# Performance work log

Measured on AMD Instinct MI355X. Metric: run time of the kernel, lower is better.

The kernel has to match this reference:

```python
import jax, jax.numpy as jnp
import numpy as np

ALPHA = 0.2  # LeakyReLU negative slope
NEG_INF = -1.0e12


def setup_inputs() -> dict:
    key = jax.random.key(0)
    ks = jax.random.split(key, 8)
    N, F, D, H, M, Q = 4096, 512, 64, 4, 2, 128
    x = jax.random.normal(ks[0], (N, F), dtype=jnp.float32)
    adj = jax.random.randint(ks[1], (M, N, N), 0, 2, dtype=jnp.int32)
    W = jax.random.normal(ks[2], (H, F, D), dtype=jnp.float32) * 0.07
    a1 = jax.random.normal(ks[3], (H, D), dtype=jnp.float32) * 0.15
    a2 = jax.random.normal(ks[4], (H, D), dtype=jnp.float32) * 0.15
    Ws = jax.random.normal(ks[5], (H * D, Q), dtype=jnp.float32) * 0.1
    bs = jax.random.normal(ks[6], (1, Q), dtype=jnp.float32) * 0.1
    q_sem = jax.random.normal(ks[7], (Q, 1), dtype=jnp.float32) * 0.15
    return {"x": x, "adj": adj, "W": W, "a1": a1, "a2": a2,
            "Ws": Ws, "bs": bs, "q_sem": q_sem}


def reference(x, adj, W, a1, a2, Ws, bs, q_sem):
    N = x.shape[0]
    # Wh is identical across meta-paths (dropout disabled / eval mode)
    Wh = jnp.einsum('nf,hfd->hnd', x, W)            # [H,N,D]
    s1 = jnp.einsum('hnd,hd->hn', Wh, a1)           # Wh @ a[:D]
    s2 = jnp.einsum('hnd,hd->hn', Wh, a2)           # Wh @ a[D:]

    def metapath(adj_m):
        # e[h,i,j] = leaky_relu(s1[h,i] + s2[h,j]); mask by adjacency
        e = jax.nn.leaky_relu(s1[:, :, None] + s2[:, None, :], negative_slope=ALPHA)
        e = jnp.where(adj_m[None, :, :] > 0, e, NEG_INF)
        att = jax.nn.softmax(e, axis=2)             # softmax over neighbors (dim=1 in torch [N,N])
        h = jax.nn.elu(jnp.einsum('hnm,hmd->hnd', att, Wh))
        return jnp.transpose(h, (1, 0, 2)).reshape(N, -1)  # concat heads -> [N, H*D]

    Z = jax.vmap(metapath)(adj)                     # [M, N, H*D]
    z = jnp.transpose(Z, (1, 0, 2))                 # [N, M, H*D]

    # Semantic attention (faithful to original, incl. softmax over dim=1 of [M,1])
    Whs = jnp.tanh(jnp.einsum('nmf,fq->nmq', z, Ws) + bs)   # [N,M,Q]
    w = jnp.einsum('nmq,qo->nmo', Whs, q_sem).mean(0)        # [M,1]
    beta = jax.nn.softmax(w, axis=1)                          # [M,1]
    return (beta[None, :, :] * z).sum(axis=1)                 # [N, H*D]
```

## Files before the change

### kernel.cpp

```cpp
#include <hip/hip_runtime.h>
#include <hip/hip_fp16.h>
#include <stdint.h>

#define NN 4096
#define FF 512
#define DD 64
#define HH 4
#define MM 2
#define LOG2E 1.44269504088896340736f
#define ALPHA_LR 0.2f

typedef float f32x4 __attribute__((ext_vector_type(4)));
typedef _Float16 f16x8 __attribute__((ext_vector_type(8)));
typedef _Float16 f16x2 __attribute__((ext_vector_type(2)));

extern "C" __device__ _Float16 __ocml_exp2_f16(_Float16);

union H4 { ushort4 u; _Float16 h[4]; };
union W8 { f16x8 v; uint32_t w[4]; f16x2 p[4]; };

__device__ inline float fast_exp2(float x) { return __builtin_amdgcn_exp2f(x); }
__device__ inline float fast_rcp(float x) { return __builtin_amdgcn_rcpf(x); }
__device__ inline f32x4 mfma16(f16x8 a, f16x8 b, f32x4 c) {
    return __builtin_amdgcn_mfma_f32_16x16x32_f16(a, b, c, 0, 0, 0);
}
__device__ inline uint32_t enc_f32(float f) {
    uint32_t u = __float_as_uint(f);
    return (u & 0x80000000u) ? ~u : (u | 0x80000000u);
}
__device__ inline float dec_f32(uint32_t k) {
    uint32_t u = (k & 0x80000000u) ? (k ^ 0x80000000u) : ~k;
    return __uint_as_float(u);
}
__device__ inline uint32_t mpair(uint32_t rs, int k) {
    return (((rs >> (2 * k)) & 1u) ? 0x0000FFFFu : 0u) |
           (((rs >> (2 * k + 1)) & 1u) ? 0xFFFF0000u : 0u);
}

__global__ __launch_bounds__(256) void k_prep(const float* __restrict__ x,
                                              const int* __restrict__ adj,
                                              const float* __restrict__ W,
                                              _Float16* __restrict__ xh,
                                              _Float16* __restrict__ wt,
                                              unsigned long long* __restrict__ bitsT,
                                              uint32_t* __restrict__ m4a) {
    const int bid = blockIdx.x;
    if (bid < 2048) {
        const long long total = (long long)MM * NN * NN;
        const long long stride = 2048LL * 256;
        long long tid = (long long)bid * 256 + threadIdx.x;
        for (long long e = tid; e < total; e += stride) {
            unsigned long long msk = __ballot(adj[e] != 0);
            if ((threadIdx.x & 63) == 0) {
                long long q = e >> 6;
                int m  = (int)(q >> 18);
                int rem = (int)(q & 262143);
                int i  = rem >> 6;
                int jw = rem & 63;
                bitsT[((size_t)m * 64 + jw) * NN + i] = msk;
            }
        }
    } else if (bid < 4096) {
        int t = (bid - 2048) * 256 + threadIdx.x;
        if (t < HH) m4a[t] = 0u;
        float4 v = ((const float4*)x)[t];
        H4 o;
        o.h[0] = (_Float16)v.x; o.h[1] = (_Float16)v.y;
        o.h[2] = (_Float16)v.z; o.h[3] = (_Float16)v.w;
        ((ushort4*)xh)[t] = o.u;
    } else {
        int t = (bid - 4096) * 256 + threadIdx.x;
        int c = t >> 9, f = t & 511;
        int h = c >> 6, d = c & 63;
        wt[t] = (_Float16)W[(h * FF + f) * DD + d];
    }
}

__global__ __launch_bounds__(512) void k_wh(const _Float16* __restrict__ xh,
                                            const _Float16* __restrict__ wt,
                                            const float* __restrict__ a1,
                                            const float* __restrict__ a2,
                                            _Float16* __restrict__ whT,
                                            float* __restrict__ s1L,
                                            _Float16* __restrict__ s2h,
                                            uint32_t* __restrict__ m4a) {
    __shared__ float sred[8][2][16];
    const int wave = threadIdx.x >> 6;
    const int h    = wave & 3;
    const int th   = wave >> 2;
    const int lane = threadIdx.x & 63;
    const int iL   = lane & 15;
    const int quad = lane >> 4;
    const int i0   = blockIdx.x * 16;

    f32x4 acc[2];
    acc[0] = (f32x4){0.f, 0.f, 0.f, 0.f};
    acc[1] = (f32x4){0.f, 0.f, 0.f, 0.f};

    const _Float16* arow  = xh + (size_t)(i0 + iL) * FF + quad * 8;
    const _Float16* bbase = wt + (size_t)(h * 64 + th * 32 + iL) * FF + quad * 8;

    for (int kc = 0; kc < FF; kc += 32) {
        f16x8 a = *(const f16x8*)(arow + kc);
        #pragma unroll
        for (int u = 0; u < 2; ++u) {
            f16x8 b = *(const f16x8*)(bbase + (size_t)(16 * u) * FF + kc);
            acc[u] = mfma16(a, b, acc[u]);
        }
    }
    #pragma unroll
    for (int u = 0; u < 2; ++u) {
        H4 o;
        #pragma unroll
        for (int r = 0; r < 4; ++r) o.h[r] = (_Float16)acc[u][r];
        *(ushort4*)(whT + (size_t)(h * 64 + th * 32 + 16 * u + iL) * NN + i0 + quad * 4) = o.u;
    }

    const float a1v0 = a1[h * 64 + th * 32 + iL];
    const float a1v1 = a1[h * 64 + th * 32 + 16 + iL];
    const float a2v0 = a2[h * 64 + th * 32 + iL];
    const float a2v1 = a2[h * 64 + th * 32 + 16 + iL];
    #pragma unroll
    for (int r = 0; r < 4; ++r) {
        float p1 = acc[0][r] * a1v0 + acc[1][r] * a1v1;
        float p2 = acc[0][r] * a2v0 + acc[1][r] * a2v1;
        #pragma unroll
        for (int off = 1; off < 16; off <<= 1) {
            p1 += __shfl_xor(p1, off);
            p2 += __shfl_xor(p2, off);
        }
        if (iL == 0) {
            sred[wave][0][quad * 4 + r] = p1;
            sred[wave][1][quad * 4 + r] = p2;
        }
    }
    __syncthreads();
    if (threadIdx.x < 64) {
        int h2  = threadIdx.x >> 4;
        int idx = threadIdx.x & 15;
        float s1 = sred[h2][0][idx] + sred[h2 + 4][0][idx];
        float s2 = sred[h2][1][idx] + sred[h2 + 4][1][idx];
        float s2l = s2 * LOG2E;
        s1L[h2 * NN + i0 + idx] = s1 * LOG2E;
        s2h[h2 * NN + i0 + idx] = (_Float16)s2l;
        float mx = s2l;
        #pragma unroll
        for (int off = 1; off < 16; off <<= 1) mx = fmaxf(mx, __shfl_xor(mx, off));
        if (idx == 0) atomicMax(m4a + h2, enc_f32(mx));
    }
}

__global__ __launch_bounds__(512, 2) void k_attn(const _Float16* __restrict__ whT,
                                                 const float* __restrict__ s1L,
                                                 const _Float16* __restrict__ s2h,
                                                 const uint32_t* __restrict__ m4a,
                                                 const unsigned long long* __restrict__ bitsT,
                                                 float* __restrict__ out) {
    __shared__ __align__(16) float xr[4][MM][4][16][16];
    __shared__ __align__(16) float dr[4][MM][16];

    const int tid  = threadIdx.x;
    const int wave = tid >> 6;
    const int lane = tid & 63;
    const int iL   = lane & 15;
    const int quad = lane >> 4;
    const int h    = blockIdx.x & 3;
    const int i0   = (blockIdx.x >> 2) * 64;

    const float m4 = dec_f32(m4a[h]);
    f16x2 A2[4], B2[4];
    #pragma unroll
    for (int s = 0; s < 4; ++s) {
        float s1i = s1L[h * NN + i0 + 16 * s + iL];
        float vv  = s1i + m4;
        float cii = fmaxf(vv, ALPHA_LR * vv);
        _Float16 a = (_Float16)(s1i - cii);
        _Float16 b = (_Float16)(ALPHA_LR * s1i - cii);
        A2[s] = (f16x2){a, a};
        B2[s] = (f16x2){b, b};
    }
    const f16x2 al2 = (f16x2){(_Float16)ALPHA_LR, (_Float16)ALPHA_LR};

    f32x4 acc[4][MM][4];
    f32x4 accD[4][MM];
    #pragma unroll
    for (int s = 0; s < 4; ++s)
        #pragma unroll
        for (int m = 0; m < MM; ++m) {
            accD[s][m] = (f32x4){0.f, 0.f, 0.f, 0.f};
            #pragma unroll
            for (int t = 0; t < 4; ++t) acc[s][m][t] = (f32x4){0.f, 0.f, 0.f, 0.f};
        }

    f16x8 bones;
    #pragma unroll
    for (int e = 0; e < 8; ++e) bones[e] = (_Float16)1.0f;

    const _Float16* s2row = s2h + h * NN;
    const _Float16* brow = whT + (size_t)(h * 64 + iL) * NN;
    const int qshift = quad * 8;
    const int jbase = wave * 512;

    const unsigned long long* pB[MM][4];
    #pragma unroll
    for (int m = 0; m < MM; ++m)
        #pragma unroll
        for (int s = 0; s < 4; ++s)
            pB[m][s] = bitsT + (size_t)m * 64 * NN + i0 + 16 * s + iL;

    for (int it = 0; it < 8; ++it) {
        const int jc = jbase + it * 64;
        const int jw = jc >> 6;
        unsigned long long bm[MM][4];
        #pragma unroll
        for (int m = 0; m < MM; ++m)
            #pragma unroll
            for (int s = 0; s < 4; ++s)
                bm[m][s] = pB[m][s][(size_t)jw * NN];

        #pragma unroll
        for (int half = 0; half < 2; ++half) {
            const int jb = jc + 32 * half;
            f16x8 bfr[4];
            #pragma unroll
            for (int t = 0; t < 4; ++t)
                bfr[t] = *(const f16x8*)(brow + (size_t)(16 * t) * NN + jb + qshift);

            const W8 s2v = *(const W8*)(s2row + jb + qshift);
            const int shft = 32 * half + qshift;

            #pragma unroll
            for (int s = 0; s < 4; ++s) {
                uint32_t rs0 = (uint32_t)(bm[0][s] >> shft);
                uint32_t rs1 = (uint32_t)(bm[1][s] >> shft);
                W8 a0, a1v;
                #pragma unroll
                for (int k = 0; k < 4; ++k) {
                    f16x2 z = s2v.p[k] + A2[s];
                    f16x2 l = al2 * s2v.p[k] + B2[s];
                    _Float16 m0 = z[0] > l[0] ? z[0] : l[0];
                    _Float16 m1 = z[1] > l[1] ? z[1] : l[1];
                    f16x2 p = (f16x2){__ocml_exp2_f16(m0), __ocml_exp2_f16(m1)};
                    uint32_t pw = __builtin_bit_cast(uint32_t, p);
                    a0.w[k]  = pw & mpair(rs0, k);
                    a1v.w[k] = pw & mpair(rs1, k);
                }
                #pragma unroll
                for (int t = 0; t < 4; ++t) {
                    acc[s][0][t] = mfma16(a0.v, bfr[t], acc[s][0][t]);
                    acc[s][1][t] = mfma16(a1v.v, bfr[t], acc[s][1][t]);
                }
                accD[s][0] = mfma16(a0.v, bones, accD[s][0]);
                accD[s][1] = mfma16(a1v.v, bones, accD[s][1]);
            }
        }
    }

    #define STORE_SLOT(sl, s)                                                 \
        { _Pragma("unroll") for (int m = 0; m < MM; ++m) {                    \
              _Pragma("unroll") for (int t = 0; t < 4; ++t)                   \
                  *(f32x4*)&xr[sl][m][t][iL][quad * 4] = acc[s][m][t];        \
              if (iL == 0) *(f32x4*)&dr[sl][m][quad * 4] = accD[s][m]; } }
    #define ADD_SLOT(sl, s)                                                   \
        { _Pragma("unroll") for (int m = 0; m < MM; ++m) {                    \
              _Pragma("unroll") for (int t = 0; t < 4; ++t)                   \
                  acc[s][m][t] += *(const f32x4*)&xr[sl][m][t][iL][quad * 4]; \
              accD[s][m] += *(const f32x4*)&dr[sl][m][quad * 4]; } }

    for (int s = 0; s < 4; ++s) {
        __syncthreads();
        if (wave >= 4) STORE_SLOT(wave - 4, s);
        __syncthreads();
        if (wave < 4) ADD_SLOT(wave, s);
        __syncthreads();
        if (wave >= 2 && wave < 4) STORE_SLOT(wave - 2, s);
        __syncthreads();
        if (wave < 2) ADD_SLOT(wave, s);
        __syncthreads();
        if (wave == 1) STORE_SLOT(0, s);
        __syncthreads();
        if (wave == 0) {
            ADD_SLOT(0, s);
            const int i0s = i0 + 16 * s;
            #pragma unroll
            for (int t = 0; t < 4; ++t) {
                #pragma unroll
                for (int r = 0; r < 4; ++r) {
                    float v0 = acc[s][0][t][r] * fast_rcp(accD[s][0][r]);
                    float v1 = acc[s][1][t][r] * fast_rcp(accD[s][1][r]);
                    float e0 = v0 > 0.f ? v0 : (fast_exp2(v0 * LOG2E) - 1.f);
                    float e1 = v1 > 0.f ? v1 : (fast_exp2(v1 * LOG2E) - 1.f);
                    out[(size_t)(i0s + quad * 4 + r) * (HH * DD) + h * 64 + 16 * t + iL] = e0 + e1;
                }
            }
        }
    }
    #undef STORE_SLOT
    #undef ADD_SLOT
}

extern "C" void kernel_launch(void* const* d_in, const int* in_sizes, int n_in,
                              void* d_out, int out_size, void* d_ws, size_t ws_size,
                              hipStream_t stream) {
    const float* x   = (const float*)d_in[0];
    const int*   adj = (const int*)d_in[1];
    const float* W   = (const float*)d_in[2];
    const float* a1  = (const float*)d_in[3];
    const float* a2  = (const float*)d_in[4];
    float* out = (float*)d_out;

    char* ws = (char*)d_ws;
    _Float16* xh   = (_Float16*)(ws);
    _Float16* wt   = (_Float16*)(ws + 4194304);
    _Float16* whT  = (_Float16*)(ws + 4456448);
    float*    s1L  = (float*)(ws + 6553600);
    _Float16* s2h  = (_Float16*)(ws + 6619136);
    uint32_t* m4a  = (uint32_t*)(ws + 6684672);
    unsigned long long* bitsT = (unsigned long long*)(ws + 6750208);

    hipLaunchKernelGGL(k_prep, dim3(4608), dim3(256), 0, stream,
                       x, adj, W, xh, wt, bitsT, m4a);
    hipLaunchKernelGGL(k_wh, dim3(256), dim3(512), 0, stream,
                       xh, wt, a1, a2, whT, s1L, s2h, m4a);
    hipLaunchKernelGGL(k_attn, dim3(256), dim3(512), 0, stream,
                       whT, s1L, s2h, m4a, bitsT, out);
}
```

Before: 276.1 us.

## Packed f16 max and mask-multiply, single-pass LDS cross-wave reduction

The inner loop now applies the adjacency mask by multiplying with packed 0/1 half values built from shifted bits, and uses a packed f16 max, replacing scalar selects and per-element AND masks. The epilogue changes from a tree reduction over waves with six barriers per slot to a single pass. All eight waves write their partials to a larger LDS buffer, and four waves each sum one output tile. This cuts barriers and serialized reduction work but doubles the LDS used for the reduction buffer, which may affect occupancy.

```diff
diff --git a/kernel.cpp b/kernel.cpp
--- a/kernel.cpp
+++ b/kernel.cpp
@@ -13,6 +13,7 @@
 typedef float f32x4 __attribute__((ext_vector_type(4)));
 typedef _Float16 f16x8 __attribute__((ext_vector_type(8)));
 typedef _Float16 f16x2 __attribute__((ext_vector_type(2)));
+typedef unsigned short u16x2 __attribute__((ext_vector_type(2)));
 
 extern "C" __device__ _Float16 __ocml_exp2_f16(_Float16);
 
@@ -32,9 +33,17 @@
     uint32_t u = (k & 0x80000000u) ? (k ^ 0x80000000u) : ~k;
     return __uint_as_float(u);
 }
-__device__ inline uint32_t mpair(uint32_t rs, int k) {
-    return (((rs >> (2 * k)) & 1u) ? 0x0000FFFFu : 0u) |
-           (((rs >> (2 * k + 1)) & 1u) ? 0xFFFF0000u : 0u);
+__device__ inline f16x2 msk01(uint32_t V, int k) {
+    uint32_t w = (V >> (2 * k)) & 0x00010001u;
+    u16x2 m = __builtin_bit_cast(u16x2, w) * (u16x2){0x3C00, 0x3C00};
+    return __builtin_bit_cast(f16x2, m);
+}
+__device__ inline f16x2 pkmax(f16x2 a, f16x2 b) {
+#if __has_builtin(__builtin_elementwise_max)
+    return __builtin_elementwise_max(a, b);
+#else
+    return (f16x2){a[0] > b[0] ? a[0] : b[0], a[1] > b[1] ? a[1] : b[1]};
+#endif
 }
 
 __global__ __launch_bounds__(256) void k_prep(const float* __restrict__ x,
@@ -156,8 +165,8 @@
                                                  const uint32_t* __restrict__ m4a,
                                                  const unsigned long long* __restrict__ bitsT,
                                                  float* __restrict__ out) {
-    __shared__ __align__(16) float xr[4][MM][4][16][16];
-    __shared__ __align__(16) float dr[4][MM][16];
+    __shared__ __align__(16) float xr[8][MM][4][16][16];
+    __shared__ __align__(16) float dr[8][MM][16];
 
     const int tid  = threadIdx.x;
     const int wave = tid >> 6;
@@ -231,19 +240,19 @@
 
             #pragma unroll
             for (int s = 0; s < 4; ++s) {
-                uint32_t rs0 = (uint32_t)(bm[0][s] >> shft);
-                uint32_t rs1 = (uint32_t)(bm[1][s] >> shft);
+                uint32_t rs0 = (uint32_t)(bm[0][s] >> shft) & 0xFFu;
+                uint32_t rs1 = (uint32_t)(bm[1][s] >> shft) & 0xFFu;
+                uint32_t V0 = rs0 | (rs0 << 15);
+                uint32_t V1 = rs1 | (rs1 << 15);
                 W8 a0, a1v;
                 #pragma unroll
                 for (int k = 0; k < 4; ++k) {
                     f16x2 z = s2v.p[k] + A2[s];
                     f16x2 l = al2 * s2v.p[k] + B2[s];
-                    _Float16 m0 = z[0] > l[0] ? z[0] : l[0];
-                    _Float16 m1 = z[1] > l[1] ? z[1] : l[1];
-                    f16x2 p = (f16x2){__ocml_exp2_f16(m0), __ocml_exp2_f16(m1)};
-                    uint32_t pw = __builtin_bit_cast(uint32_t, p);
-                    a0.w[k]  = pw & mpair(rs0, k);
-                    a1v.w[k] = pw & mpair(rs1, k);
+                    f16x2 mx = pkmax(z, l);
+                    f16x2 p = (f16x2){__ocml_exp2_f16(mx[0]), __ocml_exp2_f16(mx[1])};
+                    a0.p[k]  = p * msk01(V0, k);
+                    a1v.p[k] = p * msk01(V1, k);
                 }
                 #pragma unroll
                 for (int t = 0; t < 4; ++t) {
@@ -256,47 +265,40 @@
         }
     }
 
-    #define STORE_SLOT(sl, s)                                                 \
-        { _Pragma("unroll") for (int m = 0; m < MM; ++m) {                    \
-              _Pragma("unroll") for (int t = 0; t < 4; ++t)                   \
-                  *(f32x4*)&xr[sl][m][t][iL][quad * 4] = acc[s][m][t];        \
-              if (iL == 0) *(f32x4*)&dr[sl][m][quad * 4] = accD[s][m]; } }
-    #define ADD_SLOT(sl, s)                                                   \
-        { _Pragma("unroll") for (int m = 0; m < MM; ++m) {                    \
-              _Pragma("unroll") for (int t = 0; t < 4; ++t)                   \
-                  acc[s][m][t] += *(const f32x4*)&xr[sl][m][t][iL][quad * 4]; \
-              accD[s][m] += *(const f32x4*)&dr[sl][m][quad * 4]; } }
-
     for (int s = 0; s < 4; ++s) {
         __syncthreads();
-        if (wave >= 4) STORE_SLOT(wave - 4, s);
+        #pragma unroll
+        for (int m = 0; m < MM; ++m) {
+            #pragma unroll
+            for (int t = 0; t < 4; ++t)
+                *(f32x4*)&xr[wave][m][t][iL][quad * 4] = acc[s][m][t];
+            if (iL == 0) *(f32x4*)&dr[wave][m][quad * 4] = accD[s][m];
+        }
         __syncthreads();
-        if (wave < 4) ADD_SLOT(wave, s);
-        __syncthreads();
-        if (wave >= 2 && wave < 4) STORE_SLOT(wave - 2, s);
-        __syncthreads();
-        if (wave < 2) ADD_SLOT(wave, s);
-        __syncthreads();
-        if (wave == 1) STORE_SLOT(0, s);
-        __syncthreads();
-        if (wave == 0) {
-            ADD_SLOT(0, s);
+        if (wave < 4) {
+            const int t = wave;
+            f32x4 n0 = (f32x4){0.f, 0.f, 0.f, 0.f};
+            f32x4 n1 = (f32x4){0.f, 0.f, 0.f, 0.f};
+            f32x4 d0 = (f32x4){0.f, 0.f, 0.f, 0.f};
+            f32x4 d1 = (f32x4){0.f, 0.f, 0.f, 0.f};
+            #pragma unroll
+            for (int sl = 0; sl < 8; ++sl) {
+                n0 += *(const f32x4*)&xr[sl][0][t][iL][quad * 4];
+                n1 += *(const f32x4*)&xr[sl][1][t][iL][quad * 4];
+                d0 += *(const f32x4*)&dr[sl][0][quad * 4];
+                d1 += *(const f32x4*)&dr[sl][1][quad * 4];
+            }
             const int i0s = i0 + 16 * s;
             #pragma unroll
-            for (int t = 0; t < 4; ++t) {
-                #pragma unroll
-                for (int r = 0; r < 4; ++r) {
-                    float v0 = acc[s][0][t][r] * fast_rcp(accD[s][0][r]);
-                    float v1 = acc[s][1][t][r] * fast_rcp(accD[s][1][r]);
-                    float e0 = v0 > 0.f ? v0 : (fast_exp2(v0 * LOG2E) - 1.f);
-                    float e1 = v1 > 0.f ? v1 : (fast_exp2(v1 * LOG2E) - 1.f);
-                    out[(size_t)(i0s + quad * 4 + r) * (HH * DD) + h * 64 + 16 * t + iL] = e0 + e1;
-                }
+            for (int r = 0; r < 4; ++r) {
+                float v0 = n0[r] * fast_rcp(d0[r]);
+                float v1 = n1[r] * fast_rcp(d1[r]);
+                float e0 = v0 > 0.f ? v0 : (fast_exp2(v0 * LOG2E) - 1.f);
+                float e1 = v1 > 0.f ? v1 : (fast_exp2(v1 * LOG2E) - 1.f);
+                out[(size_t)(i0s + quad * 4 + r) * (HH * DD) + h * 64 + 16 * t + iL] = e0 + e1;
             }
         }
     }
-    #undef STORE_SLOT
-    #undef ADD_SLOT
 }
 
 extern "C" void kernel_launch(void* const* d_in, const int* in_sizes, int n_in,
```

Result: faster. 268.8 us (-2.6%).
